# Performance work log

Measured on AMD Instinct MI355X. Metric: run time of the kernel, lower is better.

Reference implementation:

```python
import jax, jax.numpy as jnp
import numpy as np

B, S, D, H, DH = 2, 2048, 1024, 16, 64
SCALE = float(np.sqrt(DH))
IGNORE = -100000.0


def setup_inputs() -> dict:
    key = jax.random.key(0)
    ks = jax.random.split(key, 9)
    s = 0.02
    return {
        "x": jax.random.normal(ks[0], (B, S, D), dtype=jnp.float32),
        "W_Q": jax.random.normal(ks[1], (H, DH, D), dtype=jnp.float32) * s,
        "W_K": jax.random.normal(ks[2], (H, DH, D), dtype=jnp.float32) * s,
        "W_V": jax.random.normal(ks[3], (H, DH, D), dtype=jnp.float32) * s,
        "W_O": jax.random.normal(ks[4], (H, D, DH), dtype=jnp.float32) * s,
        "b_Q": jax.random.normal(ks[5], (H, DH), dtype=jnp.float32) * s,
        "b_K": jax.random.normal(ks[6], (H, DH), dtype=jnp.float32) * s,
        "b_V": jax.random.normal(ks[7], (H, DH), dtype=jnp.float32) * s,
        "b_O": jax.random.normal(ks[8], (D,), dtype=jnp.float32) * s,
        "mask": jnp.tril(jnp.ones((S, S), dtype=bool)),  # causal, global attn_type
    }


def reference(x, W_Q, W_K, W_V, W_O, b_Q, b_K, b_V, b_O, mask):
    # q,k,v: [batch, pos, head, d_head]
    q = jnp.einsum('ihm,bpm->bpih', W_Q, x) + b_Q
    k = jnp.einsum('ihm,bpm->bpih', W_K, x) + b_K
    v = jnp.einsum('ihm,bpm->bpih', W_V, x) + b_V
    # scores: [batch, head, q_pos, k_pos]
    attn_scores = jnp.einsum('bpih,bqih->bipq', q, k) / SCALE
    attn_scores = jnp.where(mask, attn_scores, IGNORE)
    attn = jax.nn.softmax(attn_scores, axis=-1)
    # z: [batch, q_pos, head, d_head]
    z = jnp.einsum('bpih,biqp->bqih', v, attn)
    out = jnp.einsum('idh,bqih->bqd', W_O, z) + b_O
    return out
```

## Files before the change

kernel.cpp:

```cpp
#include <hip/hip_runtime.h>
#include <stdint.h>

typedef __attribute__((ext_vector_type(8))) short bf16x8;
typedef __attribute__((ext_vector_type(4))) float f32x4;
typedef __attribute__((ext_vector_type(16))) float f32x16;
typedef __attribute__((ext_vector_type(4))) unsigned short us4;

#define LOG2E 1.44269504088896340736f

__device__ __forceinline__ unsigned short f2bf(float f) {
    union { float f; unsigned u; } v; v.f = f;
    unsigned r = v.u + 0x7FFFu + ((v.u >> 16) & 1u);
    return (unsigned short)(r >> 16);
}
__device__ __forceinline__ float bf2f(unsigned short u) {
    return __uint_as_float(((unsigned)u) << 16);
}

__device__ __forceinline__ unsigned cvtpk(float lo, float hi) {
    unsigned r;
    asm("v_cvt_pk_bf16_f32 %0, %1, %2" : "=v"(r) : "v"(lo), "v"(hi));
    return r;
}
__device__ __forceinline__ void plswap(unsigned &a, unsigned &b) {
    asm volatile("v_permlane32_swap_b32 %0, %1" : "+v"(a), "+v"(b));
}

__device__ __forceinline__ void gld16(const void* g, void* l) {
    __builtin_amdgcn_global_load_lds((const __attribute__((address_space(1))) void*)g,
                                     (__attribute__((address_space(3))) void*)l, 16, 0, 0);
}

__global__ void k_cvt(const float* __restrict__ in, unsigned short* __restrict__ out, int n4) {
    int i = blockIdx.x * blockDim.x + threadIdx.x;
    if (i >= n4) return;
    float4 v = ((const float4*)in)[i];
    us4 o; o.x = f2bf(v.x); o.y = f2bf(v.y); o.z = f2bf(v.z); o.w = f2bf(v.w);
    *(us4*)(out + (size_t)i * 4) = o;
}

__global__ void k_cvt_wo(const float* __restrict__ WO, unsigned short* __restrict__ out) {
    int t = blockIdx.x * blockDim.x + threadIdx.x;
    int d = t >> 10, nn = t & 1023, i = nn >> 6, h = nn & 63;
    out[t] = f2bf(WO[(((size_t)i << 10) + d) * 64 + h]);
}

__global__ __launch_bounds__(256) void k_gemm_qkv(
    const unsigned short* __restrict__ Xb,
    const unsigned short* __restrict__ Wq, const unsigned short* __restrict__ Wk,
    const unsigned short* __restrict__ Wv,
    const float* __restrict__ bQ, const float* __restrict__ bK, const float* __restrict__ bV,
    unsigned short* __restrict__ Qb, unsigned short* __restrict__ Kb, unsigned short* __restrict__ VTb)
{
    __shared__ unsigned short As[128][64];
    __shared__ unsigned short Bs[128][64];
    const int which = blockIdx.z;
    const unsigned short* Wp = which == 0 ? Wq : (which == 1 ? Wk : Wv);
    const int bm = blockIdx.x, bn = blockIdx.y;
    const int t = threadIdx.x, lane = t & 63, wave = t >> 6;
    const int wm = wave >> 1, wn = wave & 1;
    const int l15 = lane & 15, l4 = lane >> 4;
    const int rsw = l15 & 7;
    f32x4 acc[4][4] = {};
    for (int k0 = 0; k0 < 1024; k0 += 64) {
        #pragma unroll
        for (int it = 0; it < 4; ++it) {
            int c = it * 256 + wave * 64 + lane;
            int row = c >> 3, sl = (c & 7) ^ (row & 7);
            gld16(Xb + ((bm << 7) + row) * 1024 + k0 + sl * 8, (char*)As + ((it * 256 + wave * 64) << 4));
            gld16(Wp + ((bn << 7) + row) * 1024 + k0 + sl * 8, (char*)Bs + ((it * 256 + wave * 64) << 4));
        }
        __syncthreads();
        const char* Ab = (const char*)As;
        const char* Bb = (const char*)Bs;
        #pragma unroll
        for (int kk = 0; kk < 2; ++kk) {
            bf16x8 af[4], bfg[4];
            #pragma unroll
            for (int m = 0; m < 4; ++m)
                af[m] = *(const bf16x8*)(Ab + (wm * 64 + m * 16 + l15) * 128 + (((kk * 4 + l4) ^ rsw) << 4));
            #pragma unroll
            for (int n = 0; n < 4; ++n)
                bfg[n] = *(const bf16x8*)(Bb + (wn * 64 + n * 16 + l15) * 128 + (((kk * 4 + l4) ^ rsw) << 4));
            #pragma unroll
            for (int m = 0; m < 4; ++m)
                #pragma unroll
                for (int n = 0; n < 4; ++n)
                    acc[m][n] = __builtin_amdgcn_mfma_f32_16x16x32_bf16(af[m], bfg[n], acc[m][n], 0, 0, 0);
        }
        __syncthreads();
    }
    #pragma unroll
    for (int m = 0; m < 4; ++m) {
        #pragma unroll
        for (int n = 0; n < 4; ++n) {
            int col = (bn << 7) + wn * 64 + n * 16 + l15;
            int i = col >> 6, h = col & 63;
            float bias = which == 0 ? bQ[col] : (which == 1 ? bK[col] : bV[col]);
            #pragma unroll
            for (int r = 0; r < 4; ++r) {
                int p = (bm << 7) + wm * 64 + m * 16 + (l4 << 2) + r;
                int b = p >> 11, s = p & 2047;
                float v = acc[m][n][r] + bias;
                if (which == 0)
                    Qb[(((((size_t)b << 4) + i) << 11) + s) * 64 + h] = f2bf(v * (0.125f * LOG2E));
                else if (which == 1)
                    Kb[(((((size_t)b << 4) + i) << 11) + s) * 64 + h] = f2bf(v);
                else
                    VTb[(((((size_t)b << 4) + i) << 6) + h) * 2048 + s] = f2bf(v);
            }
        }
    }
}

__global__ __launch_bounds__(128) void k_attn(
    const unsigned short* __restrict__ Qb, const unsigned short* __restrict__ Kb,
    const unsigned short* __restrict__ VTb,
    unsigned short* __restrict__ Zp, float* __restrict__ Lse)
{
    __shared__ __align__(16) char Lbuf[16384];
    const int id = (int)blockIdx.x;
    const int bi = id & 31;
    const int r = id >> 5;
    const int c = 31 - (r >> 1);
    const int part = r & 1;
    const int n = c + 1, n0 = (n + 1) >> 1;
    const int t0 = part ? n0 : 0, t1 = part ? n : n0;
    const int lane = threadIdx.x & 63, w = threadIdx.x >> 6;
    const int l31 = lane & 31, hi = lane >> 5;
    const unsigned short* Qh = Qb + (size_t)bi * 2048 * 64;
    const char* Khb = (const char*)(Kb + (size_t)bi * 2048 * 64);
    const char* Vhb = (const char*)(VTb + (size_t)bi * 64 * 2048);
    const int q0 = c * 64 + w * 32;
    const int q = q0 + l31;

    bf16x8 qf[4];
    #pragma unroll
    for (int kk = 0; kk < 4; ++kk)
        qf[kk] = *(const bf16x8*)&Qh[(size_t)q * 64 + kk * 16 + hi * 8];

    const int r8 = lane >> 3;
    const int swz = ((lane & 7) * 16) ^ (r8 << 4);
    const int koff = r8 * 128 + swz;
    const int voff = r8 * 4096 + swz;

    const int rsw = (l31 & 7) << 4;
    int kaddr[8];
    #pragma unroll
    for (int i = 0; i < 8; ++i)
        kaddr[i] = (l31 + 32 * (i >> 2)) * 128 + ((32 * (i & 3) + 16 * hi) ^ rsw);
    int vcol[4];
    #pragma unroll
    for (int f = 0; f < 4; ++f)
        vcol[f] = ((f * 32 + 16 * hi) ^ rsw);

    f32x16 za0 = {}, za1 = {};
    float m_run = -1e30f, l_run = 0.f;

    if (t0 < t1) {
        if (w == 0) {
            const char* src = Khb + (size_t)t0 * 8192 + koff;
            #pragma unroll
            for (int it = 0; it < 8; ++it) gld16(src + it * 1024, &Lbuf[0] + it * 1024);
        } else {
            const char* src = Vhb + (size_t)t0 * 128 + voff;
            #pragma unroll
            for (int it = 0; it < 8; ++it) gld16(src + it * 32768, &Lbuf[8192] + it * 1024);
        }
    }

    for (int t = t0; t < t1; ++t) {
        __syncthreads();
        const char* KL = &Lbuf[0];
        const char* VL = &Lbuf[8192];
        bf16x8 ka[8];
        #pragma unroll
        for (int i = 0; i < 8; ++i) ka[i] = *(const bf16x8*)(KL + kaddr[i]);
        bf16x8 vf0[4], vf1[4];
        #pragma unroll
        for (int f = 0; f < 4; ++f) {
            vf0[f] = *(const bf16x8*)(VL + l31 * 128 + vcol[f]);
            vf1[f] = *(const bf16x8*)(VL + (l31 + 32) * 128 + vcol[f]);
        }
        __syncthreads();
        if (t + 1 < t1) {
            if (w == 0) {
                const char* src = Khb + (size_t)(t + 1) * 8192 + koff;
                #pragma unroll
                for (int it = 0; it < 8; ++it) gld16(src + it * 1024, &Lbuf[0] + it * 1024);
            } else {
                const char* src = Vhb + (size_t)(t + 1) * 128 + voff;
                #pragma unroll
                for (int it = 0; it < 8; ++it) gld16(src + it * 32768, &Lbuf[8192] + it * 1024);
            }
        }

        const bool full = !(t == c && w == 0);
        f32x16 s0 = {}, s1;
        __builtin_amdgcn_s_setprio(1);
        #pragma unroll
        for (int kk = 0; kk < 4; ++kk)
            s0 = __builtin_amdgcn_mfma_f32_32x32x16_bf16(ka[kk], qf[kk], s0, 0, 0, 0);
        if (full) {
            f32x16 z = {};
            #pragma unroll
            for (int kk = 0; kk < 4; ++kk)
                z = __builtin_amdgcn_mfma_f32_32x32x16_bf16(ka[4 + kk], qf[kk], z, 0, 0, 0);
            s1 = z;
        }
        __builtin_amdgcn_s_setprio(0);

        if (!full) {
            #pragma unroll
            for (int j = 0; j < 16; ++j) s1[j] = -100000.0f;
        }
        if (t == c) {
            #pragma unroll
            for (int j = 0; j < 16; ++j) {
                int kv0 = (j & 3) + 8 * (j >> 2) + 4 * hi;
                if (c * 64 + kv0 > q) s0[j] = -100000.0f;
                if (c * 64 + kv0 + 32 > q) s1[j] = -100000.0f;
            }
        }
        float tmax = -1e30f;
        #pragma unroll
        for (int j = 0; j < 16; ++j) tmax = fmaxf(tmax, fmaxf(s0[j], s1[j]));
        tmax = fmaxf(tmax, __shfl_xor(tmax, 32, 64));
        if (!__all(tmax <= m_run + 8.0f)) {
            float newm = fmaxf(m_run, tmax);
            float alpha = exp2f(m_run - newm);
            m_run = newm;
            l_run *= alpha;
            za0 *= alpha; za1 *= alpha;
        }
        float rsum = 0.f;
        #pragma unroll
        for (int j = 0; j < 16; ++j) { s0[j] = exp2f(s0[j] - m_run); rsum += s0[j]; }
        if (full) {
            #pragma unroll
            for (int j = 0; j < 16; ++j) { s1[j] = exp2f(s1[j] - m_run); rsum += s1[j]; }
        }
        rsum += __shfl_xor(rsum, 32, 64);
        l_run += rsum;

        union { unsigned u[4]; bf16x8 v; } pk0, pk1, pk2, pk3;
        {
            unsigned a0 = cvtpk(s0[0], s0[1]),  a1 = cvtpk(s0[2], s0[3]);
            unsigned a2 = cvtpk(s0[4], s0[5]),  a3 = cvtpk(s0[6], s0[7]);
            plswap(a0, a2); plswap(a1, a3);
            pk0.u[0] = a0; pk0.u[1] = a1; pk0.u[2] = a2; pk0.u[3] = a3;
            unsigned b0 = cvtpk(s0[8], s0[9]),  b1 = cvtpk(s0[10], s0[11]);
            unsigned b2 = cvtpk(s0[12], s0[13]), b3 = cvtpk(s0[14], s0[15]);
            plswap(b0, b2); plswap(b1, b3);
            pk1.u[0] = b0; pk1.u[1] = b1; pk1.u[2] = b2; pk1.u[3] = b3;
        }
        if (full) {
            unsigned a0 = cvtpk(s1[0], s1[1]),  a1 = cvtpk(s1[2], s1[3]);
            unsigned a2 = cvtpk(s1[4], s1[5]),  a3 = cvtpk(s1[6], s1[7]);
            plswap(a0, a2); plswap(a1, a3);
            pk2.u[0] = a0; pk2.u[1] = a1; pk2.u[2] = a2; pk2.u[3] = a3;
            unsigned b0 = cvtpk(s1[8], s1[9]),  b1 = cvtpk(s1[10], s1[11]);
            unsigned b2 = cvtpk(s1[12], s1[13]), b3 = cvtpk(s1[14], s1[15]);
            plswap(b0, b2); plswap(b1, b3);
            pk3.u[0] = b0; pk3.u[1] = b1; pk3.u[2] = b2; pk3.u[3] = b3;
        }
        __builtin_amdgcn_s_setprio(1);
        za0 = __builtin_amdgcn_mfma_f32_32x32x16_bf16(vf0[0], pk0.v, za0, 0, 0, 0);
        za1 = __builtin_amdgcn_mfma_f32_32x32x16_bf16(vf1[0], pk0.v, za1, 0, 0, 0);
        za0 = __builtin_amdgcn_mfma_f32_32x32x16_bf16(vf0[1], pk1.v, za0, 0, 0, 0);
        za1 = __builtin_amdgcn_mfma_f32_32x32x16_bf16(vf1[1], pk1.v, za1, 0, 0, 0);
        if (full) {
            za0 = __builtin_amdgcn_mfma_f32_32x32x16_bf16(vf0[2], pk2.v, za0, 0, 0, 0);
            za1 = __builtin_amdgcn_mfma_f32_32x32x16_bf16(vf1[2], pk2.v, za1, 0, 0, 0);
            za0 = __builtin_amdgcn_mfma_f32_32x32x16_bf16(vf0[3], pk3.v, za0, 0, 0, 0);
            za1 = __builtin_amdgcn_mfma_f32_32x32x16_bf16(vf1[3], pk3.v, za1, 0, 0, 0);
        }
        __builtin_amdgcn_s_setprio(0);
    }

    const float rl = (l_run > 0.f) ? 1.0f / l_run : 0.f;
    const float lse = (l_run > 0.f) ? m_run + log2f(l_run) : -1e30f;
    const int pb = (part << 5) + bi;
    unsigned short* zp = Zp + ((size_t)pb * 2048 + q) * 64;
    #pragma unroll
    for (int nn = 0; nn < 2; ++nn) {
        #pragma unroll
        for (int gg = 0; gg < 4; ++gg) {
            int dh0 = nn * 32 + 8 * gg + 4 * hi;
            us4 o;
            float v0 = (nn ? za1[4 * gg + 0] : za0[4 * gg + 0]) * rl;
            float v1 = (nn ? za1[4 * gg + 1] : za0[4 * gg + 1]) * rl;
            float v2 = (nn ? za1[4 * gg + 2] : za0[4 * gg + 2]) * rl;
            float v3 = (nn ? za1[4 * gg + 3] : za0[4 * gg + 3]) * rl;
            o.x = f2bf(v0); o.y = f2bf(v1); o.z = f2bf(v2); o.w = f2bf(v3);
            *(us4*)(zp + dh0) = o;
        }
    }
    if (hi == 0) Lse[(size_t)pb * 2048 + q] = lse;
}

__global__ __launch_bounds__(256) void k_combine(
    const unsigned short* __restrict__ Zp, const float* __restrict__ Lse,
    unsigned short* __restrict__ Zb)
{
    const int tid = blockIdx.x * 256 + threadIdx.x;
    const int dc = tid & 7, q = (tid >> 3) & 2047, bi = tid >> 14;
    const float l0 = Lse[(size_t)bi * 2048 + q];
    const float l1 = Lse[(size_t)(32 + bi) * 2048 + q];
    const float M = fmaxf(l0, l1);
    float e0 = exp2f(l0 - M), e1 = exp2f(l1 - M);
    const float rs = 1.0f / (e0 + e1);
    e0 *= rs; e1 *= rs;
    const size_t base = ((size_t)bi * 2048 + q) * 64 + dc * 8;
    bf16x8 z0 = *(const bf16x8*)(Zp + base);
    bf16x8 z1 = *(const bf16x8*)(Zp + (size_t)32 * 2048 * 64 + base);
    const int b = bi >> 4, ih = bi & 15;
    unsigned short* op = Zb + (((size_t)b * 2048 + q) << 10) + ih * 64 + dc * 8;
    bf16x8 o;
    #pragma unroll
    for (int j = 0; j < 8; ++j) {
        float v = e0 * bf2f((unsigned short)z0[j]) + e1 * bf2f((unsigned short)z1[j]);
        o[j] = (short)f2bf(v);
    }
    *(bf16x8*)op = o;
}

__global__ __launch_bounds__(256) void k_gemm_out(
    const unsigned short* __restrict__ Zb, const unsigned short* __restrict__ Wo,
    const float* __restrict__ bO, float* __restrict__ out)
{
    __shared__ unsigned short As[128][64];
    __shared__ unsigned short Bs[128][64];
    const int bm = blockIdx.x, bn = blockIdx.y;
    const int t = threadIdx.x, lane = t & 63, wave = t >> 6;
    const int wm = wave >> 1, wn = wave & 1;
    const int l15 = lane & 15, l4 = lane >> 4;
    const int rsw = l15 & 7;
    f32x4 acc[4][4] = {};
    for (int k0 = 0; k0 < 1024; k0 += 64) {
        #pragma unroll
        for (int it = 0; it < 4; ++it) {
            int c = it * 256 + wave * 64 + lane;
            int row = c >> 3, sl = (c & 7) ^ (row & 7);
            gld16(Zb + ((bm << 7) + row) * 1024 + k0 + sl * 8, (char*)As + ((it * 256 + wave * 64) << 4));
            gld16(Wo + ((bn << 7) + row) * 1024 + k0 + sl * 8, (char*)Bs + ((it * 256 + wave * 64) << 4));
        }
        __syncthreads();
        const char* Ab = (const char*)As;
        const char* Bb = (const char*)Bs;
        #pragma unroll
        for (int kk = 0; kk < 2; ++kk) {
            bf16x8 af[4], bfg[4];
            #pragma unroll
            for (int m = 0; m < 4; ++m)
                af[m] = *(const bf16x8*)(Ab + (wm * 64 + m * 16 + l15) * 128 + (((kk * 4 + l4) ^ rsw) << 4));
            #pragma unroll
            for (int n = 0; n < 4; ++n)
                bfg[n] = *(const bf16x8*)(Bb + (wn * 64 + n * 16 + l15) * 128 + (((kk * 4 + l4) ^ rsw) << 4));
            #pragma unroll
            for (int m = 0; m < 4; ++m)
                #pragma unroll
                for (int n = 0; n < 4; ++n)
                    acc[m][n] = __builtin_amdgcn_mfma_f32_16x16x32_bf16(af[m], bfg[n], acc[m][n], 0, 0, 0);
        }
        __syncthreads();
    }
    #pragma unroll
    for (int m = 0; m < 4; ++m) {
        #pragma unroll
        for (int n = 0; n < 4; ++n) {
            int col = (bn << 7) + wn * 64 + n * 16 + l15;
            float bias = bO[col];
            #pragma unroll
            for (int r = 0; r < 4; ++r) {
                int p = (bm << 7) + wm * 64 + m * 16 + (l4 << 2) + r;
                out[(size_t)p * 1024 + col] = acc[m][n][r] + bias;
            }
        }
    }
}

extern "C" void kernel_launch(void* const* d_in, const int* in_sizes, int n_in,
                              void* d_out, int out_size, void* d_ws, size_t ws_size,
                              hipStream_t stream)
{
    const float* x  = (const float*)d_in[0];
    const float* WQ = (const float*)d_in[1];
    const float* WK = (const float*)d_in[2];
    const float* WV = (const float*)d_in[3];
    const float* WO = (const float*)d_in[4];
    const float* bQ = (const float*)d_in[5];
    const float* bK = (const float*)d_in[6];
    const float* bV = (const float*)d_in[7];
    const float* bO = (const float*)d_in[8];
    float* out = (float*)d_out;

    char* w = (char*)d_ws;
    unsigned short* xb  = (unsigned short*)w; w += (size_t)4096 * 1024 * 2;
    unsigned short* wqb = (unsigned short*)w; w += (size_t)1024 * 1024 * 2;
    unsigned short* wkb = (unsigned short*)w; w += (size_t)1024 * 1024 * 2;
    unsigned short* wvb = (unsigned short*)w; w += (size_t)1024 * 1024 * 2;
    unsigned short* wob = (unsigned short*)w; w += (size_t)1024 * 1024 * 2;
    unsigned short* Qb  = (unsigned short*)w; w += (size_t)4096 * 1024 * 2;
    unsigned short* Kb  = (unsigned short*)w; w += (size_t)4096 * 1024 * 2;
    unsigned short* VTb = (unsigned short*)w; w += (size_t)4096 * 1024 * 2;
    unsigned short* Zb  = (unsigned short*)w; w += (size_t)4096 * 1024 * 2;
    unsigned short* Zp  = (unsigned short*)w; w += (size_t)2 * 32 * 2048 * 64 * 2;
    float*          Lse = (float*)w;          w += (size_t)2 * 32 * 2048 * 4;

    k_cvt<<<4096, 256, 0, stream>>>(x, xb, 1048576);
    k_cvt<<<1024, 256, 0, stream>>>(WQ, wqb, 262144);
    k_cvt<<<1024, 256, 0, stream>>>(WK, wkb, 262144);
    k_cvt<<<1024, 256, 0, stream>>>(WV, wvb, 262144);
    k_cvt_wo<<<4096, 256, 0, stream>>>(WO, wob);

    k_gemm_qkv<<<dim3(32, 8, 3), 256, 0, stream>>>(xb, wqb, wkb, wvb, bQ, bK, bV, Qb, Kb, VTb);
    k_attn<<<2048, 128, 0, stream>>>(Qb, Kb, VTb, Zp, Lse);
    k_combine<<<2048, 256, 0, stream>>>(Zp, Lse, Zb);
    k_gemm_out<<<dim3(32, 8), 256, 0, stream>>>(Zb, wob, bO, out);
}
```

Measured before the change: 141.1 us.

## Double GEMM K-tile to 128, raise MFMA priority, merge weight conversions

Both the QKV and output-projection GEMMs now stage 128-wide K tiles in LDS (64 KB per block) instead of 64, halving the number of load/barrier iterations, and wrap the MFMA block in s_setprio to favour matrix issue. The three separate Q/K/V weight-conversion launches are merged into one 2D-grid kernel to cut launch overhead. Larger LDS use may reduce blocks resident per CU, and there is still no double buffering, so load latency is still exposed each iteration.

Measured after the change: 129.9 us. 1.09x faster.

```diff
diff --git a/kernel.cpp b/kernel.cpp
--- a/kernel.cpp
+++ b/kernel.cpp
@@ -34,6 +34,18 @@
 __global__ void k_cvt(const float* __restrict__ in, unsigned short* __restrict__ out, int n4) {
     int i = blockIdx.x * blockDim.x + threadIdx.x;
     if (i >= n4) return;
+    float4 v = ((const float4*)in)[i];
+    us4 o; o.x = f2bf(v.x); o.y = f2bf(v.y); o.z = f2bf(v.z); o.w = f2bf(v.w);
+    *(us4*)(out + (size_t)i * 4) = o;
+}
+
+__global__ void k_cvt3(const float* __restrict__ a, const float* __restrict__ b,
+                       const float* __restrict__ cc,
+                       unsigned short* __restrict__ oa, unsigned short* __restrict__ ob,
+                       unsigned short* __restrict__ oc) {
+    const float* in = blockIdx.y == 0 ? a : (blockIdx.y == 1 ? b : cc);
+    unsigned short* out = blockIdx.y == 0 ? oa : (blockIdx.y == 1 ? ob : oc);
+    int i = blockIdx.x * blockDim.x + threadIdx.x;
     float4 v = ((const float4*)in)[i];
     us4 o; o.x = f2bf(v.x); o.y = f2bf(v.y); o.z = f2bf(v.z); o.w = f2bf(v.w);
     *(us4*)(out + (size_t)i * 4) = o;
@@ -52,8 +64,8 @@
     const float* __restrict__ bQ, const float* __restrict__ bK, const float* __restrict__ bV,
     unsigned short* __restrict__ Qb, unsigned short* __restrict__ Kb, unsigned short* __restrict__ VTb)
 {
-    __shared__ unsigned short As[128][64];
-    __shared__ unsigned short Bs[128][64];
+    __shared__ unsigned short As[128][128];
+    __shared__ unsigned short Bs[128][128];
     const int which = blockIdx.z;
     const unsigned short* Wp = which == 0 ? Wq : (which == 1 ? Wk : Wv);
     const int bm = blockIdx.x, bn = blockIdx.y;
@@ -61,32 +73,37 @@
     const int wm = wave >> 1, wn = wave & 1;
     const int l15 = lane & 15, l4 = lane >> 4;
     const int rsw = l15 & 7;
+    const int c0 = wave * 64 + lane;
+    const int arow = bm << 7, brow = bn << 7;
     f32x4 acc[4][4] = {};
-    for (int k0 = 0; k0 < 1024; k0 += 64) {
-        #pragma unroll
-        for (int it = 0; it < 4; ++it) {
-            int c = it * 256 + wave * 64 + lane;
-            int row = c >> 3, sl = (c & 7) ^ (row & 7);
-            gld16(Xb + ((bm << 7) + row) * 1024 + k0 + sl * 8, (char*)As + ((it * 256 + wave * 64) << 4));
-            gld16(Wp + ((bn << 7) + row) * 1024 + k0 + sl * 8, (char*)Bs + ((it * 256 + wave * 64) << 4));
+
+    for (int k0 = 0; k0 < 1024; k0 += 128) {
+        #pragma unroll
+        for (int it = 0; it < 8; ++it) {
+            int c = it * 256 + c0;
+            int row = c >> 4, sl = (c & 15) ^ (row & 7);
+            gld16(Xb + ((size_t)(arow + row)) * 1024 + k0 + sl * 8, (char*)As + (c << 4));
+            gld16(Wp + ((size_t)(brow + row)) * 1024 + k0 + sl * 8, (char*)Bs + (c << 4));
         }
         __syncthreads();
         const char* Ab = (const char*)As;
         const char* Bb = (const char*)Bs;
         #pragma unroll
-        for (int kk = 0; kk < 2; ++kk) {
+        for (int kk = 0; kk < 4; ++kk) {
             bf16x8 af[4], bfg[4];
             #pragma unroll
             for (int m = 0; m < 4; ++m)
-                af[m] = *(const bf16x8*)(Ab + (wm * 64 + m * 16 + l15) * 128 + (((kk * 4 + l4) ^ rsw) << 4));
+                af[m] = *(const bf16x8*)(Ab + (wm * 64 + m * 16 + l15) * 256 + (((kk * 4 + l4) ^ rsw) << 4));
             #pragma unroll
             for (int n = 0; n < 4; ++n)
-                bfg[n] = *(const bf16x8*)(Bb + (wn * 64 + n * 16 + l15) * 128 + (((kk * 4 + l4) ^ rsw) << 4));
+                bfg[n] = *(const bf16x8*)(Bb + (wn * 64 + n * 16 + l15) * 256 + (((kk * 4 + l4) ^ rsw) << 4));
+            __builtin_amdgcn_s_setprio(1);
             #pragma unroll
             for (int m = 0; m < 4; ++m)
                 #pragma unroll
                 for (int n = 0; n < 4; ++n)
                     acc[m][n] = __builtin_amdgcn_mfma_f32_16x16x32_bf16(af[m], bfg[n], acc[m][n], 0, 0, 0);
+            __builtin_amdgcn_s_setprio(0);
         }
         __syncthreads();
     }
@@ -329,39 +346,44 @@
     const unsigned short* __restrict__ Zb, const unsigned short* __restrict__ Wo,
     const float* __restrict__ bO, float* __restrict__ out)
 {
-    __shared__ unsigned short As[128][64];
-    __shared__ unsigned short Bs[128][64];
+    __shared__ unsigned short As[128][128];
+    __shared__ unsigned short Bs[128][128];
     const int bm = blockIdx.x, bn = blockIdx.y;
     const int t = threadIdx.x, lane = t & 63, wave = t >> 6;
     const int wm = wave >> 1, wn = wave & 1;
     const int l15 = lane & 15, l4 = lane >> 4;
     const int rsw = l15 & 7;
+    const int c0 = wave * 64 + lane;
+    const int arow = bm << 7, brow = bn << 7;
     f32x4 acc[4][4] = {};
-    for (int k0 = 0; k0 < 1024; k0 += 64) {
-        #pragma unroll
-        for (int it = 0; it < 4; ++it) {
-            int c = it * 256 + wave * 64 + lane;
-            int row = c >> 3, sl = (c & 7) ^ (row & 7);
-            gld16(Zb + ((bm << 7) + row) * 1024 + k0 + sl * 8, (char*)As + ((it * 256 + wave * 64) << 4));
-            gld16(Wo + ((bn << 7) + row) * 1024 + k0 + sl * 8, (char*)Bs + ((it * 256 + wave * 64) << 4));
+
+    for (int k0 = 0; k0 < 1024; k0 += 128) {
+        #pragma unroll
+        for (int it = 0; it < 8; ++it) {
+            int c = it * 256 + c0;
+            int row = c >> 4, sl = (c & 15) ^ (row & 7);
+            gld16(Zb + ((size_t)(arow + row)) * 1024 + k0 + sl * 8, (char*)As + (c << 4));
+            gld16(Wo + ((size_t)(brow + row)) * 1024 + k0 + sl * 8, (char*)Bs + (c << 4));
         }
         __syncthreads();
         const char* Ab = (const char*)As;
         const char* Bb = (const char*)Bs;
         #pragma unroll
-        for (int kk = 0; kk < 2; ++kk) {
+        for (int kk = 0; kk < 4; ++kk) {
             bf16x8 af[4], bfg[4];
             #pragma unroll
             for (int m = 0; m < 4; ++m)
-                af[m] = *(const bf16x8*)(Ab + (wm * 64 + m * 16 + l15) * 128 + (((kk * 4 + l4) ^ rsw) << 4));
+                af[m] = *(const bf16x8*)(Ab + (wm * 64 + m * 16 + l15) * 256 + (((kk * 4 + l4) ^ rsw) << 4));
             #pragma unroll
             for (int n = 0; n < 4; ++n)
-                bfg[n] = *(const bf16x8*)(Bb + (wn * 64 + n * 16 + l15) * 128 + (((kk * 4 + l4) ^ rsw) << 4));
+                bfg[n] = *(const bf16x8*)(Bb + (wn * 64 + n * 16 + l15) * 256 + (((kk * 4 + l4) ^ rsw) << 4));
+            __builtin_amdgcn_s_setprio(1);
             #pragma unroll
             for (int m = 0; m < 4; ++m)
                 #pragma unroll
                 for (int n = 0; n < 4; ++n)
                     acc[m][n] = __builtin_amdgcn_mfma_f32_16x16x32_bf16(af[m], bfg[n], acc[m][n], 0, 0, 0);
+            __builtin_amdgcn_s_setprio(0);
         }
         __syncthreads();
     }
@@ -409,9 +431,7 @@
     float*          Lse = (float*)w;          w += (size_t)2 * 32 * 2048 * 4;
 
     k_cvt<<<4096, 256, 0, stream>>>(x, xb, 1048576);
-    k_cvt<<<1024, 256, 0, stream>>>(WQ, wqb, 262144);
-    k_cvt<<<1024, 256, 0, stream>>>(WK, wkb, 262144);
-    k_cvt<<<1024, 256, 0, stream>>>(WV, wvb, 262144);
+    k_cvt3<<<dim3(1024, 3), 256, 0, stream>>>(WQ, WK, WV, wqb, wkb, wvb);
     k_cvt_wo<<<4096, 256, 0, stream>>>(WO, wob);
 
     k_gemm_qkv<<<dim3(32, 8, 3), 256, 0, stream>>>(xb, wqb, wkb, wvb, bQ, bK, bV, Qb, Kb, VTb);
```
